# Performance work log

Hardware: AMD Instinct MI355X
Metric: run time of the kernel (lower is better)

The kernel has to match this reference:

```python
import jax, jax.numpy as jnp
import numpy as np

VT = 0.026
N_FACTOR = 1.5
VD = 0.1
ALPHA = 0.0005625
TIA_GAIN = 5000000.0
KSIZE = 3
STRIDE = 1
PAD = 1


def _unfold(x, k, pad, stride):
    # torch.nn.Unfold: output [B, C*k*k, L], channel-major (C, ki, kj) ordering
    B, C, H, W = x.shape
    xp = jnp.pad(x, ((0, 0), (0, 0), (pad, pad), (pad, pad)))
    h_out = (H + 2 * pad - k) // stride + 1
    w_out = (W + 2 * pad - k) // stride + 1
    slabs = []
    for i in range(k):
        for j in range(k):
            slabs.append(xp[:, :, i:i + h_out * stride:stride, j:j + w_out * stride:stride])
    # [B, C, k*k, h_out, w_out] with (ki,kj) minor relative to C -> matches torch unfold
    p = jnp.stack(slabs, axis=2)
    return p.reshape(B, C * k * k, h_out * w_out), h_out, w_out


def _log1p_exp(x):
    return jnp.log1p(jnp.exp(jnp.clip(x, -30.0, 30.0)))


def setup_inputs() -> dict:
    key = jax.random.key(0)
    kx, kt = jax.random.split(key)
    B, C_in, H, W = 8, 32, 32, 32
    out_channels = 64
    k = C_in * KSIZE * KSIZE  # 288
    x = jax.random.normal(kx, (B, C_in, H, W), dtype=jnp.float32)
    theta = jax.random.uniform(kt, (out_channels, k), dtype=jnp.float32, minval=2.5, maxval=4.5)
    return {"x": x, "theta": theta}


def reference(x, theta):
    B = x.shape[0]
    patches, h_out, w_out = _unfold(x, KSIZE, PAD, STRIDE)  # [B, K, L]
    vg = patches[:, None, :, :]                 # [B, 1, K, L]
    th = theta[None, :, :, None]                # [1, O, K, 1]
    inv = 1.0 / (N_FACTOR * VT)
    arg1 = (vg - th) * inv
    arg2 = (vg - th - VD) * inv
    I = ALPHA * (_log1p_exp(arg1) ** 2 - _log1p_exp(arg2) ** 2)  # [B, O, K, L]
    out = I.sum(axis=2) * TIA_GAIN              # [B, O, L]
    return out.reshape(B, -1, h_out, w_out)
```

## Files before the change

### kernel.cpp

```cpp
#include <hip/hip_runtime.h>

namespace {
constexpr float INVL  = (float)(1.0 / (1.5 * 0.026) * 1.4426950408889634);
constexpr float C2L   = (float)(0.1 / (1.5 * 0.026) * 1.4426950408889634);
constexpr float CLIPL = (float)(30.0 * 1.4426950408889634);
constexpr float SCALE = (float)(0.0005625 * 5.0e6 * 0.6931471805599453 * 0.6931471805599453);
constexpr float CUT_DELTA = (float)(4.0 * (1.5 * 0.026));
}

__global__ __launch_bounds__(1024, 8) void ekv_fused(const float* __restrict__ x,
                                                     const float* __restrict__ theta,
                                                     float* __restrict__ out) {
  __shared__ float    ths[18503];
  __shared__ float    xs[1728];
  __shared__ unsigned msk[54];
  __shared__ float    red[17];

  const int blk  = blockIdx.x;
  const int wq   = blk & 1;
  const int h    = (blk >> 1) & 31;
  const int b    = blk >> 6;
  const int tid  = threadIdx.x;
  const int lane = tid & 63;
  const int wv   = tid >> 6;

  if (tid < 54) msk[tid] = 0u;

  const float4* t4 = (const float4*)theta;
  float mn = 1e30f;
#pragma unroll
  for (int t = 0; t < 4; ++t) {
    const int j  = t * 1024 + tid;
    const float4 v = t4[j];
    const int oc = j / 72;
    const int c4 = j - oc * 72;
    float* d = &ths[c4 * 257 + oc];
    d[0] = v.x * INVL; d[64] = v.y * INVL; d[128] = v.z * INVL; d[192] = v.w * INVL;
    mn = fminf(mn, fminf(fminf(v.x, v.y), fminf(v.z, v.w)));
  }
  if (tid < 512) {
    const int j  = 4096 + tid;
    const float4 v = t4[j];
    const int oc = j / 72;
    const int c4 = j - oc * 72;
    float* d = &ths[c4 * 257 + oc];
    d[0] = v.x * INVL; d[64] = v.y * INVL; d[128] = v.z * INVL; d[192] = v.w * INVL;
    mn = fminf(mn, fminf(fminf(v.x, v.y), fminf(v.z, v.w)));
  }
#pragma unroll
  for (int off = 32; off; off >>= 1) mn = fminf(mn, __shfl_down(mn, off));
  if (lane == 0) red[wv] = mn;

  for (int j = tid; j < 1728; j += 1024) {
    const int c   = j / 54;
    const int pos = j - c * 54;
    const int rr  = pos / 18;
    const int cl  = pos - rr * 18;
    const int gh  = h - 1 + rr;
    const int gw  = wq * 16 - 1 + cl;
    float v = 0.0f;
    if ((unsigned)gh < 32u && (unsigned)gw < 32u)
      v = x[((b * 32 + c) * 32 + gh) * 32 + gw];
    xs[j] = v * INVL;
  }
  __syncthreads();

  if (tid == 0) {
    float m = red[0];
#pragma unroll
    for (int q = 1; q < 16; ++q) m = fminf(m, red[q]);
    red[16] = (m - CUT_DELTA) * INVL;
  }
  __syncthreads();

  const float cutl = red[16];
  for (int j = tid; j < 1728; j += 1024) {
    if (xs[j] > cutl) {
      const int c = j / 54;
      atomicOr(&msk[j - c * 54], 1u << c);
    }
  }
  __syncthreads();

  unsigned mv[9];
#pragma unroll
  for (int p = 0; p < 9; ++p) mv[p] = msk[(p / 3) * 18 + wv + (p % 3)];

  float acc = 0.0f;
#pragma unroll
  for (int r = 0; r < 3; ++r) {
#pragma unroll
    for (int dj = 0; dj < 3; ++dj) {
      unsigned m = __builtin_amdgcn_readfirstlane(mv[r * 3 + dj]);
      const int kb = r * 3 + dj;
      const int pb = r * 18 + wv + dj;
      while (m) {
        const int c = __builtin_ctz(m);
        m &= m - 1;
        const float vgl = xs[c * 54 + pb];
        const int col   = c * 9 + kb;
        const float thl = ths[(col >> 2) * 257 + (col & 3) * 64 + lane];
        const float a1  = vgl - thl;
        const float a1c = fminf(a1, CLIPL);
        const float a2c = fminf(a1 - C2L, CLIPL);
        const float e1  = __builtin_amdgcn_exp2f(a1c);
        const float e2  = __builtin_amdgcn_exp2f(a2c);
        const float l1  = __builtin_amdgcn_logf(1.0f + e1);
        const float l2  = __builtin_amdgcn_logf(1.0f + e2);
        acc = __builtin_fmaf(l1 - l2, l1 + l2, acc);
      }
    }
  }

  __syncthreads();
  ths[lane * 16 + ((wv + lane) & 15)] = acc * SCALE;
  __syncthreads();

  const int oc2 = tid >> 4;
  const int wp  = tid & 15;
  out[((b * 64 + oc2) * 32 + h) * 32 + wq * 16 + wp] = ths[oc2 * 16 + ((wp + oc2) & 15)];
}

extern "C" void kernel_launch(void* const* d_in, const int* in_sizes, int n_in,
                              void* d_out, int out_size, void* d_ws, size_t ws_size,
                              hipStream_t stream) {
  const float* x     = (const float*)d_in[0];
  const float* theta = (const float*)d_in[1];
  float* out         = (float*)d_out;
  (void)d_ws; (void)ws_size; (void)in_sizes; (void)n_in; (void)out_size;
  hipLaunchKernelGGL(ekv_fused, dim3(512), dim3(1024), 0, stream, x, theta, out);
}
```

Before: 11.12 us.

## Process full output row per block, halving grid and theta reloads

Each block now covers a whole 32-wide output row instead of half a row, so the grid shrinks from 512 to 256 blocks. Each wave computes two output pixels, which spreads the per-block cost of staging theta into LDS over twice the work. The single-thread cutoff reduction and its barrier are replaced by every thread reducing the 16 partial minima itself, and output stores become float2. The tradeoff is fewer blocks across the 256 CUs, so each one has more serial work and the grid has less parallelism.

Result: no change. 11.13 us (+0.1%).

```diff
diff --git a/kernel.cpp b/kernel.cpp
--- a/kernel.cpp
+++ b/kernel.cpp
@@ -12,19 +12,18 @@
                                                      const float* __restrict__ theta,
                                                      float* __restrict__ out) {
   __shared__ float    ths[18503];
-  __shared__ float    xs[1728];
-  __shared__ unsigned msk[54];
-  __shared__ float    red[17];
+  __shared__ float    xs[32 * 102];
+  __shared__ unsigned msk[102];
+  __shared__ float    red[16];
 
   const int blk  = blockIdx.x;
-  const int wq   = blk & 1;
-  const int h    = (blk >> 1) & 31;
-  const int b    = blk >> 6;
+  const int h    = blk & 31;
+  const int b    = blk >> 5;
   const int tid  = threadIdx.x;
   const int lane = tid & 63;
   const int wv   = tid >> 6;
 
-  if (tid < 54) msk[tid] = 0u;
+  if (tid < 102) msk[tid] = 0u;
 
   const float4* t4 = (const float4*)theta;
   float mn = 1e30f;
@@ -51,13 +50,13 @@
   for (int off = 32; off; off >>= 1) mn = fminf(mn, __shfl_down(mn, off));
   if (lane == 0) red[wv] = mn;
 
-  for (int j = tid; j < 1728; j += 1024) {
-    const int c   = j / 54;
-    const int pos = j - c * 54;
-    const int rr  = pos / 18;
-    const int cl  = pos - rr * 18;
+  for (int j = tid; j < 3264; j += 1024) {
+    const int c   = j / 102;
+    const int pos = j - c * 102;
+    const int rr  = pos / 34;
+    const int cl  = pos - rr * 34;
     const int gh  = h - 1 + rr;
-    const int gw  = wq * 16 - 1 + cl;
+    const int gw  = cl - 1;
     float v = 0.0f;
     if ((unsigned)gh < 32u && (unsigned)gw < 32u)
       v = x[((b * 32 + c) * 32 + gh) * 32 + gw];
@@ -65,60 +64,65 @@
   }
   __syncthreads();
 
-  if (tid == 0) {
-    float m = red[0];
+  float cm = red[0];
 #pragma unroll
-    for (int q = 1; q < 16; ++q) m = fminf(m, red[q]);
-    red[16] = (m - CUT_DELTA) * INVL;
-  }
-  __syncthreads();
+  for (int q = 1; q < 16; ++q) cm = fminf(cm, red[q]);
+  const float cutl = (cm - CUT_DELTA) * INVL;
 
-  const float cutl = red[16];
-  for (int j = tid; j < 1728; j += 1024) {
+  for (int j = tid; j < 3264; j += 1024) {
     if (xs[j] > cutl) {
-      const int c = j / 54;
-      atomicOr(&msk[j - c * 54], 1u << c);
+      const int c = j / 102;
+      atomicOr(&msk[j - c * 102], 1u << c);
     }
   }
   __syncthreads();
 
-  unsigned mv[9];
+  float accs[2];
 #pragma unroll
-  for (int p = 0; p < 9; ++p) mv[p] = msk[(p / 3) * 18 + wv + (p % 3)];
-
-  float acc = 0.0f;
+  for (int px = 0; px < 2; ++px) {
+    const int w = wv + px * 16;
+    unsigned mv[9];
 #pragma unroll
-  for (int r = 0; r < 3; ++r) {
+    for (int p = 0; p < 9; ++p) mv[p] = msk[(p / 3) * 34 + w + (p % 3)];
+    float acc = 0.0f;
 #pragma unroll
-    for (int dj = 0; dj < 3; ++dj) {
-      unsigned m = __builtin_amdgcn_readfirstlane(mv[r * 3 + dj]);
-      const int kb = r * 3 + dj;
-      const int pb = r * 18 + wv + dj;
-      while (m) {
-        const int c = __builtin_ctz(m);
-        m &= m - 1;
-        const float vgl = xs[c * 54 + pb];
-        const int col   = c * 9 + kb;
-        const float thl = ths[(col >> 2) * 257 + (col & 3) * 64 + lane];
-        const float a1  = vgl - thl;
-        const float a1c = fminf(a1, CLIPL);
-        const float a2c = fminf(a1 - C2L, CLIPL);
-        const float e1  = __builtin_amdgcn_exp2f(a1c);
-        const float e2  = __builtin_amdgcn_exp2f(a2c);
-        const float l1  = __builtin_amdgcn_logf(1.0f + e1);
-        const float l2  = __builtin_amdgcn_logf(1.0f + e2);
-        acc = __builtin_fmaf(l1 - l2, l1 + l2, acc);
+    for (int r = 0; r < 3; ++r) {
+#pragma unroll
+      for (int dj = 0; dj < 3; ++dj) {
+        unsigned m = __builtin_amdgcn_readfirstlane(mv[r * 3 + dj]);
+        const int kb = r * 3 + dj;
+        const int pb = r * 34 + w + dj;
+        while (m) {
+          const int c = __builtin_ctz(m);
+          m &= m - 1;
+          const float vgl = xs[c * 102 + pb];
+          const int col   = c * 9 + kb;
+          const float thl = ths[(col >> 2) * 257 + (col & 3) * 64 + lane];
+          const float a1  = vgl - thl;
+          const float a1c = fminf(a1, CLIPL);
+          const float a2c = fminf(a1 - C2L, CLIPL);
+          const float e1  = __builtin_amdgcn_exp2f(a1c);
+          const float e2  = __builtin_amdgcn_exp2f(a2c);
+          const float l1  = __builtin_amdgcn_logf(1.0f + e1);
+          const float l2  = __builtin_amdgcn_logf(1.0f + e2);
+          acc = __builtin_fmaf(l1 - l2, l1 + l2, acc);
+        }
       }
     }
+    accs[px] = acc * SCALE;
   }
 
   __syncthreads();
-  ths[lane * 16 + ((wv + lane) & 15)] = acc * SCALE;
+  ths[lane * 33 + wv]      = accs[0];
+  ths[lane * 33 + wv + 16] = accs[1];
   __syncthreads();
 
   const int oc2 = tid >> 4;
-  const int wp  = tid & 15;
-  out[((b * 64 + oc2) * 32 + h) * 32 + wq * 16 + wp] = ths[oc2 * 16 + ((wp + oc2) & 15)];
+  const int w2  = (tid & 15) * 2;
+  float2 o;
+  o.x = ths[oc2 * 33 + w2];
+  o.y = ths[oc2 * 33 + w2 + 1];
+  *(float2*)(out + (((b * 64 + oc2) * 32 + h) * 32 + w2)) = o;
 }
 
 extern "C" void kernel_launch(void* const* d_in, const int* in_sizes, int n_in,
@@ -128,5 +132,5 @@
   const float* theta = (const float*)d_in[1];
   float* out         = (float*)d_out;
   (void)d_ws; (void)ws_size; (void)in_sizes; (void)n_in; (void)out_size;
-  hipLaunchKernelGGL(ekv_fused, dim3(512), dim3(1024), 0, stream, x, theta, out);
+  hipLaunchKernelGGL(ekv_fused, dim3(256), dim3(1024), 0, stream, x, theta, out);
 }
```
